# Kernel tuning notes

Hardware: AMD Instinct MI355X
Metric: run time of the kernel (lower is better)

The kernel has to match this reference:

```python
import jax, jax.numpy as jnp
import numpy as np

POOL_H, POOL_W = 7, 7


def _crop_and_resize(fm, boxes, box_idx, ph, pw):
    """TF tf.image.crop_and_resize (bilinear) semantics.
    fm: [B,H,W,C]; boxes: [N,4] normalized (y1,x1,y2,x2); box_idx: [N] int32.
    Returns [N,ph,pw,C]. Boxes are in [0,1] so all samples are in-bounds."""
    B, H, W, C = fm.shape
    y1, x1, y2, x2 = boxes[:, 0], boxes[:, 1], boxes[:, 2], boxes[:, 3]
    gy = jnp.arange(ph, dtype=fm.dtype)
    gx = jnp.arange(pw, dtype=fm.dtype)
    # sample coordinates per TF: y = y1*(H-1) + i*(y2-y1)*(H-1)/(ph-1)
    ys = y1[:, None] * (H - 1) + gy[None, :] * ((y2 - y1)[:, None] * (H - 1) / (ph - 1))  # [N,ph]
    xs = x1[:, None] * (W - 1) + gx[None, :] * ((x2 - x1)[:, None] * (W - 1) / (pw - 1))  # [N,pw]
    y0 = jnp.floor(ys)
    x0 = jnp.floor(xs)
    wy = (ys - y0)[:, :, None, None]  # [N,ph,1,1]
    wx = (xs - x0)[:, None, :, None]  # [N,1,pw,1]
    y0i = jnp.clip(y0, 0, H - 1).astype(jnp.int32)
    y1i = jnp.clip(y0 + 1, 0, H - 1).astype(jnp.int32)
    x0i = jnp.clip(x0, 0, W - 1).astype(jnp.int32)
    x1i = jnp.clip(x0 + 1, 0, W - 1).astype(jnp.int32)
    b = box_idx[:, None, None]
    tl = fm[b, y0i[:, :, None], x0i[:, None, :]]  # [N,ph,pw,C]
    tr = fm[b, y0i[:, :, None], x1i[:, None, :]]
    bl = fm[b, y1i[:, :, None], x0i[:, None, :]]
    br = fm[b, y1i[:, :, None], x1i[:, None, :]]
    top = tl + (tr - tl) * wx
    bot = bl + (br - bl) * wx
    return top + (bot - top) * wy


def _forward(boxes, image_meta, feat2, feat3, feat4, feat5):
    B, N, _ = boxes.shape
    h = boxes[..., 2] - boxes[..., 0]  # [B,N]
    w = boxes[..., 3] - boxes[..., 1]
    image_shape = image_meta[0, 4:7]
    image_area = image_shape[0] * image_shape[1]
    # FPN level assignment (Mask R-CNN eq.): level = 4 + log2(sqrt(h*w)/(224/sqrt(area)))
    roi_level = jnp.log2(jnp.sqrt(h * w) / (224.0 / jnp.sqrt(image_area)))
    roi_level = jnp.clip(4 + jnp.round(roi_level).astype(jnp.int32), 2, 5)  # [B,N]

    flat_boxes = jax.lax.stop_gradient(boxes.reshape(B * N, 4))  # matches tf.stop_gradient(level_boxes)
    flat_idx = jnp.repeat(jnp.arange(B, dtype=jnp.int32), N)
    levels = roi_level.reshape(B * N)

    fms = [feat2, feat3, feat4, feat5]
    # Crop every box against every level, then select per-box level (static shapes;
    # equivalent math to the original per-level gather + reassembly in box order).
    pooled_all = jnp.stack([_crop_and_resize(fm, flat_boxes, flat_idx, POOL_H, POOL_W)
                            for fm in fms])  # [4, B*N, ph, pw, C]
    onehot = (levels[None, :] == jnp.arange(2, 6, dtype=jnp.int32)[:, None]).astype(pooled_all.dtype)
    pooled = jnp.einsum('ln,lnhwc->nhwc', onehot, pooled_all)
    C = feat2.shape[-1]
    return pooled.reshape(B, N, POOL_H, POOL_W, C)


def setup_inputs() -> dict:
    key = jax.random.key(0)
    ks = jax.random.split(key, 6)
    B, N, C = 2, 1000, 256
    # valid normalized boxes: corners from two random points, min/max per axis
    pts = jax.random.uniform(ks[0], (B, N, 2, 2), dtype=jnp.float32)
    lo = jnp.min(pts, axis=2)
    hi = jnp.clip(lo + jnp.maximum(jnp.max(pts, axis=2) - lo, 1e-3), 0.0, 1.0)
    boxes = jnp.stack([lo[..., 0], lo[..., 1], hi[..., 0], hi[..., 1]], axis=-1)
    image_meta = jnp.zeros((B, 93), jnp.float32).at[:, 4:7].set(jnp.array([1024.0, 1024.0, 3.0]))
    feat2 = jax.random.normal(ks[1], (B, 256, 256, C), jnp.float32)
    feat3 = jax.random.normal(ks[2], (B, 128, 128, C), jnp.float32)
    feat4 = jax.random.normal(ks[3], (B, 64, 64, C), jnp.float32)
    feat5 = jax.random.normal(ks[4], (B, 32, 32, C), jnp.float32)
    return {"boxes": boxes, "image_meta": image_meta, "feat2": feat2,
            "feat3": feat3, "feat4": feat4, "feat5": feat5}


def reference(boxes, image_meta, feat2, feat3, feat4, feat5):
    return _forward(boxes, image_meta, feat2, feat3, feat4, feat5)
```

## Files before the change

kernel.cpp:

```cpp
#include <hip/hip_runtime.h>
#include <math.h>

#define POOL 7
#define NPOS 49
#define CCH 256

__global__ __launch_bounds__(256) void roialign_kernel(
    const float* __restrict__ boxes,
    const float* __restrict__ meta,
    const float* __restrict__ f2,
    const float* __restrict__ f3,
    const float* __restrict__ f4,
    const float* __restrict__ f5,
    float* __restrict__ out,
    int nPos, int N)
{
    const int wave = threadIdx.x >> 6;
    const int lane = threadIdx.x & 63;
    const int pos  = blockIdx.x * 4 + wave;
    if (pos >= nPos) return;

    const int box = pos / NPOS;
    const int p   = pos - box * NPOS;
    const int py  = p / POOL;
    const int px  = p - py * POOL;
    const int b   = box / N;

    const float y1 = boxes[box * 4 + 0];
    const float x1 = boxes[box * 4 + 1];
    const float y2 = boxes[box * 4 + 2];
    const float x2 = boxes[box * 4 + 3];
    const float h = y2 - y1;
    const float w = x2 - x1;

    const float area = meta[4] * meta[5];
    const float cc   = 224.0f / sqrtf(area);
    const float roi  = log2f(sqrtf(h * w) / cc);
    int lvl = 4 + (int)rintf(roi);
    lvl = min(max(lvl, 2), 5);

    const float* fm;
    int H;
    if      (lvl == 2) { fm = f2; H = 256; }
    else if (lvl == 3) { fm = f3; H = 128; }
    else if (lvl == 4) { fm = f4; H = 64;  }
    else               { fm = f5; H = 32;  }

    const float Hm1 = (float)(H - 1);
    const float step_y = h * Hm1 / 6.0f;
    const float step_x = w * Hm1 / 6.0f;
    const float ysf = y1 * Hm1 + (float)py * step_y;
    const float xsf = x1 * Hm1 + (float)px * step_x;

    const float y0f = floorf(ysf);
    const float x0f = floorf(xsf);
    const float wy = ysf - y0f;
    const float wx = xsf - x0f;

    const int y0i = min(max((int)y0f, 0), H - 1);
    const int y1i = min((int)y0f + 1, H - 1);
    const int x0i = min(max((int)x0f, 0), H - 1);
    const int x1i = min((int)x0f + 1, H - 1);

    const size_t rowT = ((size_t)b * H + (size_t)y0i) * (size_t)H;
    const size_t rowB = ((size_t)b * H + (size_t)y1i) * (size_t)H;
    const size_t c0   = (size_t)lane * 4;

    const float4 tl = *(const float4*)(fm + (rowT + x0i) * CCH + c0);
    const float4 tr = *(const float4*)(fm + (rowT + x1i) * CCH + c0);
    const float4 bl = *(const float4*)(fm + (rowB + x0i) * CCH + c0);
    const float4 br = *(const float4*)(fm + (rowB + x1i) * CCH + c0);

    float4 o;
    {
        float top, bot;
        top = tl.x + (tr.x - tl.x) * wx;  bot = bl.x + (br.x - bl.x) * wx;  o.x = top + (bot - top) * wy;
        top = tl.y + (tr.y - tl.y) * wx;  bot = bl.y + (br.y - bl.y) * wx;  o.y = top + (bot - top) * wy;
        top = tl.z + (tr.z - tl.z) * wx;  bot = bl.z + (br.z - bl.z) * wx;  o.z = top + (bot - top) * wy;
        top = tl.w + (tr.w - tl.w) * wx;  bot = bl.w + (br.w - bl.w) * wx;  o.w = top + (bot - top) * wy;
    }

    *(float4*)(out + (size_t)pos * CCH + c0) = o;
}

extern "C" void kernel_launch(void* const* d_in, const int* in_sizes, int n_in,
                              void* d_out, int out_size, void* d_ws, size_t ws_size,
                              hipStream_t stream) {
    const float* boxes = (const float*)d_in[0];
    const float* meta  = (const float*)d_in[1];
    const float* f2    = (const float*)d_in[2];
    const float* f3    = (const float*)d_in[3];
    const float* f4    = (const float*)d_in[4];
    const float* f5    = (const float*)d_in[5];
    float* out = (float*)d_out;

    const int nBoxes = in_sizes[0] / 4;
    const int B      = in_sizes[1] / 93;
    const int N      = nBoxes / B;
    const int nPos   = nBoxes * NPOS;

    const int blocks = (nPos + 3) / 4;
    roialign_kernel<<<blocks, 256, 0, stream>>>(boxes, meta, f2, f3, f4, f5, out, nPos, N);
}
```

Measured before the change: 249.0 us.

## Sort boxes by FPN level before RoIAlign and use nontemporal output stores

Adds a single-block pre-pass that buckets boxes by pyramid level into a workspace order array. The main kernel then processes boxes in level-grouped order so that concurrent waves read the same feature map, which should improve cache locality. The per-box level computation moves out of the main kernel. Output stores become nontemporal so the written results do not evict feature-map lines from cache. The trade-offs are an extra launch, a serial one-block sort using shared atomics, and one indirection through the order array.

After: 256.2 us. 2.9% more time.

```diff
diff --git a/kernel.cpp b/kernel.cpp
--- a/kernel.cpp
+++ b/kernel.cpp
@@ -5,9 +5,54 @@
 #define NPOS 49
 #define CCH 256
 
+typedef float f32x4 __attribute__((ext_vector_type(4)));
+
+__device__ __forceinline__ int compute_level(const float* __restrict__ boxes,
+                                             float cc, int box) {
+    const float y1 = boxes[box * 4 + 0];
+    const float x1 = boxes[box * 4 + 1];
+    const float y2 = boxes[box * 4 + 2];
+    const float x2 = boxes[box * 4 + 3];
+    const float h = y2 - y1;
+    const float w = x2 - x1;
+    const float roi = log2f(sqrtf(h * w) / cc);
+    int lvl = 4 + (int)rintf(roi);
+    return min(max(lvl, 2), 5);
+}
+
+__global__ __launch_bounds__(256) void level_sort_kernel(
+    const float* __restrict__ boxes, const float* __restrict__ meta,
+    int2* __restrict__ order, int nBoxes)
+{
+    __shared__ int cnt[4];
+    __shared__ int base[4];
+    __shared__ int cur[4];
+    const float area = meta[4] * meta[5];
+    const float cc = 224.0f / sqrtf(area);
+
+    if (threadIdx.x < 4) cnt[threadIdx.x] = 0;
+    __syncthreads();
+    for (int i = threadIdx.x; i < nBoxes; i += blockDim.x)
+        atomicAdd(&cnt[compute_level(boxes, cc, i) - 2], 1);
+    __syncthreads();
+    if (threadIdx.x == 0) {
+        base[0] = 0;
+        base[1] = cnt[0];
+        base[2] = cnt[0] + cnt[1];
+        base[3] = cnt[0] + cnt[1] + cnt[2];
+        cur[0] = cur[1] = cur[2] = cur[3] = 0;
+    }
+    __syncthreads();
+    for (int i = threadIdx.x; i < nBoxes; i += blockDim.x) {
+        const int l = compute_level(boxes, cc, i) - 2;
+        const int slot = base[l] + atomicAdd(&cur[l], 1);
+        order[slot] = make_int2(i, l + 2);
+    }
+}
+
 __global__ __launch_bounds__(256) void roialign_kernel(
     const float* __restrict__ boxes,
-    const float* __restrict__ meta,
+    const int2* __restrict__ order,
     const float* __restrict__ f2,
     const float* __restrict__ f3,
     const float* __restrict__ f4,
@@ -20,10 +65,14 @@
     const int pos  = blockIdx.x * 4 + wave;
     if (pos >= nPos) return;
 
-    const int box = pos / NPOS;
-    const int p   = pos - box * NPOS;
+    const int sp  = pos / NPOS;
+    const int p   = pos - sp * NPOS;
     const int py  = p / POOL;
     const int px  = p - py * POOL;
+
+    const int2 oi = order[sp];
+    const int box = oi.x;
+    const int lvl = oi.y;
     const int b   = box / N;
 
     const float y1 = boxes[box * 4 + 0];
@@ -32,12 +81,6 @@
     const float x2 = boxes[box * 4 + 3];
     const float h = y2 - y1;
     const float w = x2 - x1;
-
-    const float area = meta[4] * meta[5];
-    const float cc   = 224.0f / sqrtf(area);
-    const float roi  = log2f(sqrtf(h * w) / cc);
-    int lvl = 4 + (int)rintf(roi);
-    lvl = min(max(lvl, 2), 5);
 
     const float* fm;
     int H;
@@ -71,7 +114,7 @@
     const float4 bl = *(const float4*)(fm + (rowB + x0i) * CCH + c0);
     const float4 br = *(const float4*)(fm + (rowB + x1i) * CCH + c0);
 
-    float4 o;
+    f32x4 o;
     {
         float top, bot;
         top = tl.x + (tr.x - tl.x) * wx;  bot = bl.x + (br.x - bl.x) * wx;  o.x = top + (bot - top) * wy;
@@ -80,7 +123,8 @@
         top = tl.w + (tr.w - tl.w) * wx;  bot = bl.w + (br.w - bl.w) * wx;  o.w = top + (bot - top) * wy;
     }
 
-    *(float4*)(out + (size_t)pos * CCH + c0) = o;
+    __builtin_nontemporal_store(o, (f32x4*)(out + (size_t)box * NPOS * CCH
+                                            + (size_t)p * CCH + c0));
 }
 
 extern "C" void kernel_launch(void* const* d_in, const int* in_sizes, int n_in,
@@ -93,12 +137,16 @@
     const float* f4    = (const float*)d_in[4];
     const float* f5    = (const float*)d_in[5];
     float* out = (float*)d_out;
+    int2* order = (int2*)d_ws;
 
     const int nBoxes = in_sizes[0] / 4;
     const int B      = in_sizes[1] / 93;
     const int N      = nBoxes / B;
     const int nPos   = nBoxes * NPOS;
 
+    level_sort_kernel<<<1, 256, 0, stream>>>(boxes, meta, order, nBoxes);
+
     const int blocks = (nPos + 3) / 4;
-    roialign_kernel<<<blocks, 256, 0, stream>>>(boxes, meta, f2, f3, f4, f5, out, nPos, N);
+    roialign_kernel<<<blocks, 256, 0, stream>>>(boxes, order, f2, f3, f4, f5,
+                                                out, nPos, N);
 }
```
